# Kernel tuning notes

Measured on AMD Instinct MI355X. Metric: run time of the kernel, lower is better.

The kernel has to match this reference:

```python
import jax, jax.numpy as jnp
import numpy as np

B_GRAPHS = 64      # number of graphs in the batch
NODES_PER_G = 1600 # nodes per graph (equal-size for simplicity; math is ragged-safe via segment_sum)
N = B_GRAPHS * NODES_PER_G  # 102400 nodes
F_DIM = 128
K_CLUSTERS = 16
AVG_DEG = 32
E = N * AVG_DEG  # 3276800 edges


def setup_inputs() -> dict:
    key = jax.random.key(0)
    k1, k2, k3, k4, k5, k6 = jax.random.split(key, 6)
    x = jax.random.normal(k1, (N, F_DIM), jnp.float32)
    W = jax.random.normal(k2, (F_DIM, K_CLUSTERS), jnp.float32) * (1.0 / np.sqrt(F_DIM))
    b = jnp.zeros((K_CLUSTERS,), jnp.float32)
    # edges are constrained to lie within a graph (adjacency is block-diagonal across graphs)
    g = jax.random.randint(k3, (E,), 0, B_GRAPHS)
    edge_src = jax.random.randint(k4, (E,), 0, NODES_PER_G) + g * NODES_PER_G
    edge_dst = jax.random.randint(k5, (E,), 0, NODES_PER_G) + g * NODES_PER_G
    edge_weight = jax.random.uniform(k6, (E,), jnp.float32)
    batch = jnp.repeat(jnp.arange(B_GRAPHS), NODES_PER_G)  # sorted graph ids, as batch2ptr requires
    return {"x": x, "W": W, "b": b, "edge_weight": edge_weight,
            "edge_src": edge_src, "edge_dst": edge_dst, "batch": batch}


def reference(x, W, b, edge_weight, edge_src, edge_dst, batch):
    K = W.shape[1]
    Bn = B_GRAPHS
    n_nodes = x.shape[0]
    # forward() applies softmax once, then mincut_pool applies softmax again (temp=1.0)
    s = jax.nn.softmax(x @ W + b, axis=-1)
    s = jax.nn.softmax(s, axis=-1)                      # [N, K]
    # d = adj.sum(axis=0): column sums of the sparse adjacency
    deg = jax.ops.segment_sum(edge_weight, edge_dst, num_segments=n_nodes)  # [N]
    # M = A @ S without materializing block-diagonal C_bd:  M[i] = sum_j w_ij * s[j]
    M = jax.ops.segment_sum(edge_weight[:, None] * s[edge_dst], edge_src, num_segments=n_nodes)  # [N, K]
    # out_adj blocks: S_b^T A_b S_b  -> [B, K, K]  (C_bd^T A C_bd is block-diagonal)
    out_adj = jax.ops.segment_sum(s[:, :, None] * M[:, None, :], batch, num_segments=Bn)
    # mincut loss = -trace(C^T A C) / trace(C^T D C)
    mincut_num = jnp.sum(jnp.trace(out_adj, axis1=1, axis2=2))
    mincut_den = jnp.sum(deg * jnp.sum(s * s, axis=1))
    mincut_loss = -mincut_num / mincut_den
    # CC blocks: S_b^T S_b -> [B, K, K]
    CC = jax.ops.segment_sum(s[:, :, None] * s[:, None, :], batch, num_segments=Bn)
    cc_norm = jnp.sqrt(jnp.sum(CC * CC, axis=(1, 2)))   # per-graph Frobenius norm of CC block
    eye_div_k = jnp.eye(K, dtype=x.dtype) / jnp.sqrt(jnp.asarray(K, x.dtype))
    diff = CC / cc_norm[:, None, None] - eye_div_k
    ortho_loss = jnp.mean(jnp.sqrt(jnp.sum(diff * diff, axis=(1, 2))))
    # mask diagonal of pooled adjacency, then symmetric degree-normalize
    out_adj = out_adj * (1.0 - jnp.eye(K, dtype=x.dtype))
    d_pool = jnp.sqrt(jnp.sum(out_adj, axis=2)) + 1e-12  # [B, K] row sums -> sqrt + eps
    out_adj_n = out_adj / (d_pool[:, :, None] * d_pool[:, None, :])
    # out_x: per-graph S_b^T X_b, vstacked -> [B*K, F]; module applies SELU
    out_x = jax.ops.segment_sum(s[:, :, None] * x[:, None, :], batch, num_segments=Bn)
    out_x = jax.nn.selu(out_x.reshape(Bn * K, -1))
    return out_x, out_adj_n, mincut_loss, ortho_loss
```

## Files before the change

kernel.cpp:

```cpp
#include <hip/hip_runtime.h>
#include <math.h>

#define NN 102400
#define FD 128
#define KC 16
#define BG 64
#define NPG 1600
#define NE 3276800
#define HB 512
#define EH (NE / HB)
#define EPT (EH / 256)
#define BINS 256
#define RPB 400
#define ZTOT (16384 + 16384 + 131072 + 8 + 8)

__device__ __forceinline__ void glob_addf(float* p, float v) {
  unsafeAtomicAdd(p, v);
}
__device__ __forceinline__ unsigned f2bf(float f) {
  unsigned u = __float_as_uint(f);
  u += 0x7FFFu + ((u >> 16) & 1u);
  return (u >> 16) & 0xFFFFu;
}
__device__ __forceinline__ float bf2f(unsigned h) {
  return __uint_as_float(h << 16);
}

__global__ __launch_bounds__(256) void k_s(const float* __restrict__ x,
    const float* __restrict__ W, const float* __restrict__ bb,
    float* __restrict__ s, unsigned* __restrict__ zbase) {
  const int t = threadIdx.x;
  const int n = blockIdx.x * 256 + t;
  for (int i = n; i < ZTOT; i += NN) zbase[i] = 0u;
  float acc[KC];
#pragma unroll
  for (int k = 0; k < KC; ++k) acc[k] = bb[k];
  const float4* xr = (const float4*)(x + (size_t)n * FD);
#pragma unroll 4
  for (int c = 0; c < FD / 4; ++c) {
    float4 v = xr[c];
    const float* wr = W + c * 4 * KC;
#pragma unroll
    for (int k = 0; k < KC; ++k)
      acc[k] += v.x * wr[k] + v.y * wr[KC + k] + v.z * wr[2 * KC + k] + v.w * wr[3 * KC + k];
  }
#pragma unroll
  for (int r = 0; r < 2; ++r) {
    float m = acc[0];
#pragma unroll
    for (int k = 1; k < KC; ++k) m = fmaxf(m, acc[k]);
    float sum = 0.f;
#pragma unroll
    for (int k = 0; k < KC; ++k) { acc[k] = expf(acc[k] - m); sum += acc[k]; }
    float inv = 1.f / sum;
#pragma unroll
    for (int k = 0; k < KC; ++k) acc[k] *= inv;
  }
  float4* so = (float4*)(s + (size_t)n * KC);
  so[0] = make_float4(acc[0], acc[1], acc[2], acc[3]);
  so[1] = make_float4(acc[4], acc[5], acc[6], acc[7]);
  so[2] = make_float4(acc[8], acc[9], acc[10], acc[11]);
  so[3] = make_float4(acc[12], acc[13], acc[14], acc[15]);
}

__global__ __launch_bounds__(256) void k_hist(const int* __restrict__ esrc,
    unsigned* __restrict__ blkhist) {
  __shared__ unsigned h[BINS];
  const int t = threadIdx.x, b = blockIdx.x;
  h[t] = 0u;
  __syncthreads();
  const int e0 = b * EH;
  for (int i = t; i < EH; i += 256) {
    unsigned bin = (unsigned)esrc[e0 + i] / (unsigned)RPB;
    atomicAdd(&h[bin], 1u);
  }
  __syncthreads();
  blkhist[t * HB + b] = h[t];
}

__global__ __launch_bounds__(512) void k_scan_a(unsigned* __restrict__ blkhist,
    unsigned* __restrict__ gtot) {
  __shared__ unsigned wsum[8];
  const int t = threadIdx.x, bin = blockIdx.x;
  const int lane = t & 63;
  unsigned v = blkhist[bin * HB + t];
  unsigned inc = v;
#pragma unroll
  for (int o = 1; o < 64; o <<= 1) {
    unsigned nb = __shfl_up(inc, o, 64);
    if (lane >= o) inc += nb;
  }
  if (lane == 63) wsum[t >> 6] = inc;
  __syncthreads();
  if (t == 0) {
    unsigned run = 0;
#pragma unroll
    for (int i = 0; i < 8; ++i) { unsigned c = wsum[i]; wsum[i] = run; run += c; }
    gtot[bin] = run;
  }
  __syncthreads();
  blkhist[bin * HB + t] = inc - v + wsum[t >> 6];
}

__global__ __launch_bounds__(64) void k_scan_b(const unsigned* __restrict__ gtot,
    unsigned* __restrict__ gbase) {
  const int t = threadIdx.x;
  unsigned v0 = gtot[t * 4], v1 = gtot[t * 4 + 1];
  unsigned v2 = gtot[t * 4 + 2], v3 = gtot[t * 4 + 3];
  unsigned sum = v0 + v1 + v2 + v3;
  unsigned inc = sum;
#pragma unroll
  for (int o = 1; o < 64; o <<= 1) {
    unsigned nb = __shfl_up(inc, o, 64);
    if (t >= o) inc += nb;
  }
  unsigned ex = inc - sum;
  gbase[t * 4] = ex;
  gbase[t * 4 + 1] = ex + v0;
  gbase[t * 4 + 2] = ex + v0 + v1;
  gbase[t * 4 + 3] = ex + v0 + v1 + v2;
  if (t == 63) gbase[BINS] = inc;
}

__global__ __launch_bounds__(256, 2) void k_scatter2(const float* __restrict__ ew,
    const int* __restrict__ esrc, const int* __restrict__ edst,
    const unsigned* __restrict__ blkhist, const unsigned* __restrict__ gbase,
    unsigned short* __restrict__ skey, unsigned* __restrict__ pay) {
  __shared__ unsigned cur[BINS];
  __shared__ unsigned gadj[BINS];
  __shared__ unsigned wsum[4];
  __shared__ unsigned pays[EH];
  __shared__ unsigned gofs[EH];
  __shared__ unsigned short keys[EH];
  const int t = threadIdx.x, b = blockIdx.x;
  cur[t] = 0u;
  const unsigned gstart = gbase[t] + blkhist[t * HB + b];
  __syncthreads();
  unsigned rpay[EPT], rmeta[EPT];
  const int e0 = b * EH;
#pragma unroll
  for (int i = 0; i < EPT; ++i) {
    const int e = e0 + t + i * 256;
    int s0 = esrc[e], d0 = edst[e];
    float w = ew[e];
    unsigned bin = (unsigned)s0 / (unsigned)RPB;
    unsigned g = bin >> 2;
    rmeta[i] = (bin << 16) | ((unsigned)s0 - bin * RPB);
    rpay[i] = (((unsigned)d0 - g * NPG) << 16) | f2bf(w);
    atomicAdd(&cur[bin], 1u);
  }
  __syncthreads();
  {
    unsigned v = cur[t];
    unsigned inc = v;
#pragma unroll
    for (int o = 1; o < 64; o <<= 1) {
      unsigned nb = __shfl_up(inc, o, 64);
      if ((t & 63) >= o) inc += nb;
    }
    if ((t & 63) == 63) wsum[t >> 6] = inc;
    __syncthreads();
    if (t == 0) {
      unsigned run = 0;
#pragma unroll
      for (int i = 0; i < 4; ++i) { unsigned c = wsum[i]; wsum[i] = run; run += c; }
    }
    __syncthreads();
    const unsigned boff = inc - v + wsum[t >> 6];
    cur[t] = boff;
    gadj[t] = gstart - boff;
  }
  __syncthreads();
#pragma unroll
  for (int i = 0; i < EPT; ++i) {
    const unsigned bin = rmeta[i] >> 16;
    const unsigned pos = atomicAdd(&cur[bin], 1u);
    pays[pos] = rpay[i];
    keys[pos] = (unsigned short)(rmeta[i] & 0xFFFFu);
    gofs[pos] = gadj[bin] + pos;
  }
  __syncthreads();
  for (int p = t; p < EH; p += 256) {
    const unsigned ga = gofs[p];
    pay[ga] = pays[p];
    skey[ga] = keys[p];
  }
}

__global__ __launch_bounds__(1024, 1) void k_msc3(const float* __restrict__ s,
    const unsigned short* __restrict__ skey, const unsigned* __restrict__ pay,
    const unsigned* __restrict__ gbase, float* __restrict__ adj_raw,
    float* __restrict__ den) {
  __shared__ float SL[NPG * 17];
  __shared__ unsigned Ml[RPB * 17];
  __shared__ float P[1024];
  __shared__ float scr[16];
  const int t = threadIdx.x;
  const int bin = (blockIdx.x & 7) * 32 + (blockIdx.x >> 3);
  const int g = bin >> 2;
  const int q = bin & 3;
  const float4* sg4 = (const float4*)(s + (size_t)g * NPG * KC);
  for (int u4 = t; u4 < NPG * KC / 4; u4 += 1024) {
    float4 v = sg4[u4];
    const int u = u4 * 4;
    float* d = &SL[(u >> 4) * 17 + (u & 15)];
    d[0] = v.x; d[1] = v.y; d[2] = v.z; d[3] = v.w;
  }
  for (int i = t; i < RPB * 17; i += 1024) Ml[i] = 0u;
  __syncthreads();
  const unsigned gb = gbase[bin], ge = gbase[bin + 1];
  const int l = t & 15;
  const int gid = t >> 4;
  const float FXS = 16777216.f;
  float dacc = 0.f;
  unsigned e = gb + gid;
  for (; e + 192 < ge; e += 256) {
    unsigned pk0 = pay[e],       pk1 = pay[e + 64];
    unsigned pk2 = pay[e + 128], pk3 = pay[e + 192];
    unsigned sk0 = skey[e],       sk1 = skey[e + 64];
    unsigned sk2 = skey[e + 128], sk3 = skey[e + 192];
    float sv0 = SL[(pk0 >> 16) * 17 + l];
    float sv1 = SL[(pk1 >> 16) * 17 + l];
    float sv2 = SL[(pk2 >> 16) * 17 + l];
    float sv3 = SL[(pk3 >> 16) * 17 + l];
    float t0 = bf2f(pk0 & 0xFFFFu) * sv0;
    float t1 = bf2f(pk1 & 0xFFFFu) * sv1;
    float t2 = bf2f(pk2 & 0xFFFFu) * sv2;
    float t3 = bf2f(pk3 & 0xFFFFu) * sv3;
    dacc = fmaf(t0, sv0, dacc);
    dacc = fmaf(t1, sv1, dacc);
    dacc = fmaf(t2, sv2, dacc);
    dacc = fmaf(t3, sv3, dacc);
    atomicAdd(&Ml[sk0 * 17 + l], __float2uint_rn(t0 * FXS));
    atomicAdd(&Ml[sk1 * 17 + l], __float2uint_rn(t1 * FXS));
    atomicAdd(&Ml[sk2 * 17 + l], __float2uint_rn(t2 * FXS));
    atomicAdd(&Ml[sk3 * 17 + l], __float2uint_rn(t3 * FXS));
  }
  for (; e < ge; e += 64) {
    unsigned pk0 = pay[e];
    unsigned sk0 = skey[e];
    float sv0 = SL[(pk0 >> 16) * 17 + l];
    float t0 = bf2f(pk0 & 0xFFFFu) * sv0;
    dacc = fmaf(t0, sv0, dacc);
    atomicAdd(&Ml[sk0 * 17 + l], __float2uint_rn(t0 * FXS));
  }
  __syncthreads();
  const int ck = (t >> 4) & 15, cl = t & 15, sub = t >> 8;
  float pacc = 0.f;
  const float* SLq = SL + q * RPB * 17;
#pragma unroll 4
  for (int ii = 0; ii < RPB / 4; ++ii) {
    const int r = sub + 4 * ii;
    pacc = fmaf(SLq[r * 17 + ck], (float)Ml[r * 17 + cl], pacc);
  }
  P[t] = pacc;
#pragma unroll
  for (int o = 32; o > 0; o >>= 1) dacc += __shfl_down(dacc, o, 64);
  if ((t & 63) == 0) scr[t >> 6] = dacc;
  __syncthreads();
  if (t < 256) glob_addf(adj_raw + g * 256 + t,
                         (P[t] + P[t + 256] + P[t + 512] + P[t + 768])
                             * 5.9604644775390625e-8f);
  if (t == 0) {
    float sum = 0.f;
#pragma unroll
    for (int i = 0; i < 16; ++i) sum += scr[i];
    glob_addf(den, sum);
  }
}

__global__ __launch_bounds__(256, 8) void k_mid(const float* __restrict__ s,
    const float* __restrict__ x, float* __restrict__ cc_raw,
    float* __restrict__ outx_raw) {
  __shared__ float st[100 * KC];
  const int t = threadIdx.x;
  const int g = blockIdx.x >> 4, sub = blockIdx.x & 15;
  const int n0 = g * NPG + sub * 100;
  const int j = t & 127, h = t >> 7;
  const int kc = t >> 4, lc = t & 15;
  for (int u = t; u < 100 * KC; u += 256) st[u] = s[(size_t)n0 * KC + u];
  __syncthreads();
  float accX[8] = {0.f, 0.f, 0.f, 0.f, 0.f, 0.f, 0.f, 0.f};
  float accC = 0.f;
  for (int i = 0; i < 100; ++i) {
    const float xv = x[(size_t)(n0 + i) * FD + j];
    const float* si = st + i * KC;
#pragma unroll
    for (int kk = 0; kk < 8; ++kk) accX[kk] = fmaf(si[h * 8 + kk], xv, accX[kk]);
    accC = fmaf(si[kc], si[lc], accC);
  }
#pragma unroll
  for (int kk = 0; kk < 8; ++kk)
    glob_addf(outx_raw + g * 2048 + (h * 8 + kk) * 128 + j, accX[kk]);
  glob_addf(cc_raw + g * 256 + t, accC);
}

__device__ __forceinline__ float bred(float v, float* scr) {
#pragma unroll
  for (int o = 32; o > 0; o >>= 1) v += __shfl_down(v, o, 64);
  __syncthreads();
  if ((threadIdx.x & 63) == 0) scr[threadIdx.x >> 6] = v;
  __syncthreads();
  return scr[0] + scr[1] + scr[2] + scr[3];
}

__global__ __launch_bounds__(256) void k_post(const float* __restrict__ adj_raw,
    const float* __restrict__ cc_raw, const float* __restrict__ outx_raw,
    float* __restrict__ out, float* __restrict__ scal, unsigned* __restrict__ done) {
  const int b = blockIdx.x, t = threadIdx.x;
  const int k = t >> 4, l = t & 15;
  __shared__ float m[16 * 17];
  __shared__ float dk[16];
  __shared__ float scr[4];
  const float raw = adj_raw[b * 256 + t];
  const float masked = (k == l) ? 0.f : raw;
  m[k * 17 + l] = masked;
  __syncthreads();
  if (t < 16) {
    float rs = 0.f;
#pragma unroll
    for (int ll = 0; ll < 16; ++ll) rs += m[t * 17 + ll];
    dk[t] = sqrtf(rs) + 1e-12f;
  }
  __syncthreads();
  out[131072 + b * 256 + t] = masked / (dk[k] * dk[l]);
  float tr = bred((k == l) ? raw : 0.f, scr);
  if (t == 0) glob_addf(scal + 1, tr);
  const float c = cc_raw[b * 256 + t];
  float n2 = bred(c * c, scr);
  float diff = c / sqrtf(n2) - ((k == l) ? 0.25f : 0.f);
  float d2 = bred(diff * diff, scr);
  if (t == 0) glob_addf(scal + 2, sqrtf(d2));
  for (int idx = b * 256 + t; idx < 131072; idx += 16384) {
    float xv = outx_raw[idx];
    out[idx] = xv > 0.f ? 1.0507009873554805f * xv
                        : 1.0507009873554805f * 1.6732632423543772f * expm1f(xv);
  }
  __syncthreads();
  if (t == 0) {
    __threadfence();
    unsigned v = __hip_atomic_fetch_add(done, 1u, __ATOMIC_ACQ_REL,
                                        __HIP_MEMORY_SCOPE_AGENT);
    if (v == 63u) {
      float den   = __hip_atomic_load(scal + 0, __ATOMIC_RELAXED, __HIP_MEMORY_SCOPE_AGENT);
      float num   = __hip_atomic_load(scal + 1, __ATOMIC_RELAXED, __HIP_MEMORY_SCOPE_AGENT);
      float ortho = __hip_atomic_load(scal + 2, __ATOMIC_RELAXED, __HIP_MEMORY_SCOPE_AGENT);
      out[147456] = -num / den;
      out[147457] = ortho * (1.f / 64.f);
    }
  }
}

extern "C" void kernel_launch(void* const* d_in, const int* in_sizes, int n_in,
                              void* d_out, int out_size, void* d_ws, size_t ws_size,
                              hipStream_t stream) {
  const float* x  = (const float*)d_in[0];
  const float* W  = (const float*)d_in[1];
  const float* bb = (const float*)d_in[2];
  const float* ew = (const float*)d_in[3];
  const int* esrc = (const int*)d_in[4];
  const int* edst = (const int*)d_in[5];
  float* out = (float*)d_out;
  float* ws = (float*)d_ws;

  float* s_buf   = ws;
  float* adj_raw = s_buf + (size_t)NN * KC;
  float* cc_raw  = adj_raw + 16384;
  float* outx    = cc_raw + 16384;
  float* scal    = outx + 131072;
  unsigned* done = (unsigned*)(scal + 8);
  unsigned* gtot = done + 8;
  unsigned* gbase = gtot + BINS;
  unsigned* blkhist = gbase + 264;
  unsigned short* skey = (unsigned short*)(blkhist + (size_t)BINS * HB);
  unsigned* pay = (unsigned*)(skey + NE);

  k_s<<<NN / 256, 256, 0, stream>>>(x, W, bb, s_buf, (unsigned*)adj_raw);
  k_hist<<<HB, 256, 0, stream>>>(esrc, blkhist);
  k_scan_a<<<BINS, 512, 0, stream>>>(blkhist, gtot);
  k_scan_b<<<1, 64, 0, stream>>>(gtot, gbase);
  k_scatter2<<<HB, 256, 0, stream>>>(ew, esrc, edst, blkhist, gbase, skey, pay);
  k_msc3<<<BINS, 1024, 0, stream>>>(s_buf, skey, pay, gbase, adj_raw, scal);
  k_mid<<<BG * 16, 256, 0, stream>>>(s_buf, x, cc_raw, outx);
  k_post<<<64, 256, 0, stream>>>(adj_raw, cc_raw, outx, out, scal, done);
}
```

Baseline: 227.1 us.

## Fuse softmax, histogram and S^T X / S^T S accumulation into one kernel

Merges the per-node softmax kernel, the edge histogram kernel and the k_mid pooling kernel into a single 512-block kernel. Each block computes s for 200 nodes, keeps it in shared memory and reduces S^T X and S^T S from it. Partial sums are written to per-block buffers instead of global atomics, and k_post sums the 8 partials per graph. Workspace zeroing moves into k_scan_a. This drops two launches and a reload of s, but uses fewer, larger blocks with 56 threads idle in the softmax phase, and adds more partial-buffer traffic in k_post.

```diff
diff --git a/kernel.cpp b/kernel.cpp
--- a/kernel.cpp
+++ b/kernel.cpp
@@ -12,7 +12,7 @@
 #define EPT (EH / 256)
 #define BINS 256
 #define RPB 400
-#define ZTOT (16384 + 16384 + 131072 + 8 + 8)
+#define NPB 200
 
 __device__ __forceinline__ void glob_addf(float* p, float v) {
   unsafeAtomicAdd(p, v);
@@ -26,47 +26,16 @@
   return __uint_as_float(h << 16);
 }
 
-__global__ __launch_bounds__(256) void k_s(const float* __restrict__ x,
+__global__ __launch_bounds__(256, 4) void k_s2(const float* __restrict__ x,
     const float* __restrict__ W, const float* __restrict__ bb,
-    float* __restrict__ s, unsigned* __restrict__ zbase) {
-  const int t = threadIdx.x;
-  const int n = blockIdx.x * 256 + t;
-  for (int i = n; i < ZTOT; i += NN) zbase[i] = 0u;
-  float acc[KC];
-#pragma unroll
-  for (int k = 0; k < KC; ++k) acc[k] = bb[k];
-  const float4* xr = (const float4*)(x + (size_t)n * FD);
-#pragma unroll 4
-  for (int c = 0; c < FD / 4; ++c) {
-    float4 v = xr[c];
-    const float* wr = W + c * 4 * KC;
-#pragma unroll
-    for (int k = 0; k < KC; ++k)
-      acc[k] += v.x * wr[k] + v.y * wr[KC + k] + v.z * wr[2 * KC + k] + v.w * wr[3 * KC + k];
-  }
-#pragma unroll
-  for (int r = 0; r < 2; ++r) {
-    float m = acc[0];
-#pragma unroll
-    for (int k = 1; k < KC; ++k) m = fmaxf(m, acc[k]);
-    float sum = 0.f;
-#pragma unroll
-    for (int k = 0; k < KC; ++k) { acc[k] = expf(acc[k] - m); sum += acc[k]; }
-    float inv = 1.f / sum;
-#pragma unroll
-    for (int k = 0; k < KC; ++k) acc[k] *= inv;
-  }
-  float4* so = (float4*)(s + (size_t)n * KC);
-  so[0] = make_float4(acc[0], acc[1], acc[2], acc[3]);
-  so[1] = make_float4(acc[4], acc[5], acc[6], acc[7]);
-  so[2] = make_float4(acc[8], acc[9], acc[10], acc[11]);
-  so[3] = make_float4(acc[12], acc[13], acc[14], acc[15]);
-}
-
-__global__ __launch_bounds__(256) void k_hist(const int* __restrict__ esrc,
-    unsigned* __restrict__ blkhist) {
+    const int* __restrict__ esrc, float* __restrict__ s,
+    unsigned* __restrict__ blkhist, float* __restrict__ cc_part,
+    float* __restrict__ outx_part) {
+  __shared__ float st[NPB * KC];
   __shared__ unsigned h[BINS];
   const int t = threadIdx.x, b = blockIdx.x;
+  const int g = b >> 3, sub = b & 7;
+  const int n0 = g * NPG + sub * NPB;
   h[t] = 0u;
   __syncthreads();
   const int e0 = b * EH;
@@ -76,13 +45,64 @@
   }
   __syncthreads();
   blkhist[t * HB + b] = h[t];
+  if (t < NPB) {
+    float acc[KC];
+#pragma unroll
+    for (int k = 0; k < KC; ++k) acc[k] = bb[k];
+    const float4* xr = (const float4*)(x + (size_t)(n0 + t) * FD);
+#pragma unroll 4
+    for (int c = 0; c < FD / 4; ++c) {
+      float4 v = xr[c];
+      const float* wr = W + c * 4 * KC;
+#pragma unroll
+      for (int k = 0; k < KC; ++k)
+        acc[k] += v.x * wr[k] + v.y * wr[KC + k] + v.z * wr[2 * KC + k] + v.w * wr[3 * KC + k];
+    }
+#pragma unroll
+    for (int r = 0; r < 2; ++r) {
+      float m = acc[0];
+#pragma unroll
+      for (int k = 1; k < KC; ++k) m = fmaxf(m, acc[k]);
+      float sum = 0.f;
+#pragma unroll
+      for (int k = 0; k < KC; ++k) { acc[k] = expf(acc[k] - m); sum += acc[k]; }
+      float inv = 1.f / sum;
+#pragma unroll
+      for (int k = 0; k < KC; ++k) acc[k] *= inv;
+    }
+#pragma unroll
+    for (int k = 0; k < KC; ++k) st[t * KC + k] = acc[k];
+    float4* so = (float4*)(s + (size_t)(n0 + t) * KC);
+    so[0] = make_float4(acc[0], acc[1], acc[2], acc[3]);
+    so[1] = make_float4(acc[4], acc[5], acc[6], acc[7]);
+    so[2] = make_float4(acc[8], acc[9], acc[10], acc[11]);
+    so[3] = make_float4(acc[12], acc[13], acc[14], acc[15]);
+  }
+  __syncthreads();
+  const int j = t & 127, h2 = t >> 7;
+  const int kc = t >> 4, lc = t & 15;
+  float accX[8] = {0.f, 0.f, 0.f, 0.f, 0.f, 0.f, 0.f, 0.f};
+  float accC = 0.f;
+  for (int i = 0; i < NPB; ++i) {
+    const float xv = x[(size_t)(n0 + i) * FD + j];
+    const float* si = st + i * KC;
+#pragma unroll
+    for (int kk = 0; kk < 8; ++kk) accX[kk] = fmaf(si[h2 * 8 + kk], xv, accX[kk]);
+    accC = fmaf(si[kc], si[lc], accC);
+  }
+#pragma unroll
+  for (int kk = 0; kk < 8; ++kk)
+    outx_part[(size_t)b * 2048 + (h2 * 8 + kk) * 128 + j] = accX[kk];
+  cc_part[b * 256 + t] = accC;
 }
 
 __global__ __launch_bounds__(512) void k_scan_a(unsigned* __restrict__ blkhist,
-    unsigned* __restrict__ gtot) {
+    unsigned* __restrict__ gtot, unsigned* __restrict__ azero) {
   __shared__ unsigned wsum[8];
   const int t = threadIdx.x, bin = blockIdx.x;
   const int lane = t & 63;
+  const unsigned zi = (unsigned)bin * 512u + (unsigned)t;
+  if (zi < 16400u) azero[zi] = 0u;
   unsigned v = blkhist[bin * HB + t];
   unsigned inc = v;
 #pragma unroll
@@ -269,32 +289,6 @@
   }
 }
 
-__global__ __launch_bounds__(256, 8) void k_mid(const float* __restrict__ s,
-    const float* __restrict__ x, float* __restrict__ cc_raw,
-    float* __restrict__ outx_raw) {
-  __shared__ float st[100 * KC];
-  const int t = threadIdx.x;
-  const int g = blockIdx.x >> 4, sub = blockIdx.x & 15;
-  const int n0 = g * NPG + sub * 100;
-  const int j = t & 127, h = t >> 7;
-  const int kc = t >> 4, lc = t & 15;
-  for (int u = t; u < 100 * KC; u += 256) st[u] = s[(size_t)n0 * KC + u];
-  __syncthreads();
-  float accX[8] = {0.f, 0.f, 0.f, 0.f, 0.f, 0.f, 0.f, 0.f};
-  float accC = 0.f;
-  for (int i = 0; i < 100; ++i) {
-    const float xv = x[(size_t)(n0 + i) * FD + j];
-    const float* si = st + i * KC;
-#pragma unroll
-    for (int kk = 0; kk < 8; ++kk) accX[kk] = fmaf(si[h * 8 + kk], xv, accX[kk]);
-    accC = fmaf(si[kc], si[lc], accC);
-  }
-#pragma unroll
-  for (int kk = 0; kk < 8; ++kk)
-    glob_addf(outx_raw + g * 2048 + (h * 8 + kk) * 128 + j, accX[kk]);
-  glob_addf(cc_raw + g * 256 + t, accC);
-}
-
 __device__ __forceinline__ float bred(float v, float* scr) {
 #pragma unroll
   for (int o = 32; o > 0; o >>= 1) v += __shfl_down(v, o, 64);
@@ -305,7 +299,7 @@
 }
 
 __global__ __launch_bounds__(256) void k_post(const float* __restrict__ adj_raw,
-    const float* __restrict__ cc_raw, const float* __restrict__ outx_raw,
+    const float* __restrict__ cc_part, const float* __restrict__ outx_part,
     float* __restrict__ out, float* __restrict__ scal, unsigned* __restrict__ done) {
   const int b = blockIdx.x, t = threadIdx.x;
   const int k = t >> 4, l = t & 15;
@@ -326,13 +320,18 @@
   out[131072 + b * 256 + t] = masked / (dk[k] * dk[l]);
   float tr = bred((k == l) ? raw : 0.f, scr);
   if (t == 0) glob_addf(scal + 1, tr);
-  const float c = cc_raw[b * 256 + t];
+  float c = 0.f;
+#pragma unroll
+  for (int u = 0; u < 8; ++u) c += cc_part[(b * 8 + u) * 256 + t];
   float n2 = bred(c * c, scr);
   float diff = c / sqrtf(n2) - ((k == l) ? 0.25f : 0.f);
   float d2 = bred(diff * diff, scr);
   if (t == 0) glob_addf(scal + 2, sqrtf(d2));
   for (int idx = b * 256 + t; idx < 131072; idx += 16384) {
-    float xv = outx_raw[idx];
+    const int gg = idx >> 11, v = idx & 2047;
+    float xv = 0.f;
+#pragma unroll
+    for (int u = 0; u < 8; ++u) xv += outx_part[(size_t)(gg * 8 + u) * 2048 + v];
     out[idx] = xv > 0.f ? 1.0507009873554805f * xv
                         : 1.0507009873554805f * 1.6732632423543772f * expm1f(xv);
   }
@@ -363,24 +362,22 @@
   float* out = (float*)d_out;
   float* ws = (float*)d_ws;
 
-  float* s_buf   = ws;
-  float* adj_raw = s_buf + (size_t)NN * KC;
-  float* cc_raw  = adj_raw + 16384;
-  float* outx    = cc_raw + 16384;
-  float* scal    = outx + 131072;
-  unsigned* done = (unsigned*)(scal + 8);
-  unsigned* gtot = done + 8;
+  float* s_buf    = ws;
+  float* adj_raw  = s_buf + (size_t)NN * KC;
+  float* scal     = adj_raw + 16384;
+  unsigned* done  = (unsigned*)(scal + 8);
+  float* cc_part  = (float*)(done + 8);
+  float* outx_part= cc_part + 131072;
+  unsigned* gtot  = (unsigned*)(outx_part + 1048576);
   unsigned* gbase = gtot + BINS;
   unsigned* blkhist = gbase + 264;
   unsigned short* skey = (unsigned short*)(blkhist + (size_t)BINS * HB);
   unsigned* pay = (unsigned*)(skey + NE);
 
-  k_s<<<NN / 256, 256, 0, stream>>>(x, W, bb, s_buf, (unsigned*)adj_raw);
-  k_hist<<<HB, 256, 0, stream>>>(esrc, blkhist);
-  k_scan_a<<<BINS, 512, 0, stream>>>(blkhist, gtot);
+  k_s2<<<HB, 256, 0, stream>>>(x, W, bb, esrc, s_buf, blkhist, cc_part, outx_part);
+  k_scan_a<<<BINS, 512, 0, stream>>>(blkhist, gtot, (unsigned*)adj_raw);
   k_scan_b<<<1, 64, 0, stream>>>(gtot, gbase);
   k_scatter2<<<HB, 256, 0, stream>>>(ew, esrc, edst, blkhist, gbase, skey, pay);
   k_msc3<<<BINS, 1024, 0, stream>>>(s_buf, skey, pay, gbase, adj_raw, scal);
-  k_mid<<<BG * 16, 256, 0, stream>>>(s_buf, x, cc_raw, outx);
-  k_post<<<64, 256, 0, stream>>>(adj_raw, cc_raw, outx, out, scal, done);
-}
+  k_post<<<64, 256, 0, stream>>>(adj_raw, cc_part, outx_part, out, scal, done);
+}
```

New measurement: 218.0 us. -4.0%, faster.
